# Optimization experiments

Hardware: AMD Instinct MI355X
Metric: run time of the kernel (lower is better)

Reference implementation:

```python
import jax, jax.numpy as jnp
import numpy as np
from functools import partial

T, B, I, H, L = 2048, 64, 256, 256, 3


def setup_inputs() -> dict:
    key = jax.random.key(0)
    ks = jax.random.split(key, 5)
    s = 1.0 / np.sqrt(H)  # PyTorch-style init scale
    x = jax.random.normal(ks[0], (T, B, I), dtype=jnp.float32)
    W_ih = jax.random.normal(ks[1], (L, 3 * H, I), dtype=jnp.float32) * s
    W_hh = jax.random.normal(ks[2], (L, 3 * H, H), dtype=jnp.float32) * s
    b_ih = jax.random.normal(ks[3], (L, 3 * H), dtype=jnp.float32) * s
    b_hh = jax.random.normal(ks[4], (L, 3 * H), dtype=jnp.float32) * s
    return {"x": x, "W_ih": W_ih, "W_hh": W_hh, "b_ih": b_ih, "b_hh": b_hh}


def _gru_layer(inp, Wi, Wh, bi, bh):
    # inp: [T, B, F]; Wi: [3H, F]; Wh: [3H, H]
    H_ = Wh.shape[1]
    # Precompute input-side gates for all timesteps (big GEMM outside scan).
    gi = jnp.einsum('tbf,gf->tbg', inp, Wi) + bi  # [T, B, 3H]

    def step(h, gi_t):
        gh = jnp.einsum('bh,gh->bg', h, Wh) + bh  # [B, 3H]
        i_r, i_z, i_n = jnp.split(gi_t, 3, axis=-1)
        h_r, h_z, h_n = jnp.split(gh, 3, axis=-1)
        r = jax.nn.sigmoid(i_r + h_r)
        z = jax.nn.sigmoid(i_z + h_z)
        n = jnp.tanh(i_n + r * h_n)
        h_new = (1.0 - z) * n + z * h
        return h_new, h_new

    h0 = jnp.zeros((inp.shape[1], H_), dtype=inp.dtype)
    _, out = jax.lax.scan(step, h0, gi)  # out: [T, B, H]
    return out


def reference(x, W_ih, W_hh, b_ih, b_hh):
    out = x
    for l in range(W_ih.shape[0]):  # fixed small layer count
        out = _gru_layer(out, W_ih[l], W_hh[l], b_ih[l], b_hh[l])
    return out[-1]  # [B, H] (last timestep of top layer)
```

## Files before the change

### kernel.cpp

```cpp
#include <hip/hip_runtime.h>
#include <cstdint>
#include <cstddef>

#define NT 2048
#define NB 64
#define NH 256
#define NG 768
#define NL 3
#define CHUNK 128
#define NCH (NT / CHUNK)

typedef _Float16 h2 __attribute__((ext_vector_type(2)));
union HU { unsigned int u; h2 h; };

__device__ __forceinline__ float sigf(float x) {
    return 1.0f / (1.0f + __expf(-x));
}
__device__ __forceinline__ float tanhfast(float x) {
    float e = __expf(2.0f * x);
    return 1.0f - 2.0f / (e + 1.0f);
}

__device__ __forceinline__ float dot8(uint4 wv, uint4 hv, float acc) {
#if __has_builtin(__builtin_amdgcn_fdot2)
    HU a, b;
    a.u = wv.x; b.u = hv.x; acc = __builtin_amdgcn_fdot2(a.h, b.h, acc, false);
    a.u = wv.y; b.u = hv.y; acc = __builtin_amdgcn_fdot2(a.h, b.h, acc, false);
    a.u = wv.z; b.u = hv.z; acc = __builtin_amdgcn_fdot2(a.h, b.h, acc, false);
    a.u = wv.w; b.u = hv.w; acc = __builtin_amdgcn_fdot2(a.h, b.h, acc, false);
#else
    HU a, b;
    const unsigned int wu[4] = {wv.x, wv.y, wv.z, wv.w};
    const unsigned int hu[4] = {hv.x, hv.y, hv.z, hv.w};
#pragma unroll
    for (int i = 0; i < 4; ++i) {
        a.u = wu[i]; b.u = hu[i];
        acc = fmaf((float)a.h[0], (float)b.h[0], acc);
        acc = fmaf((float)a.h[1], (float)b.h[1], acc);
    }
#endif
    return acc;
}

__global__ void repack_whh(const float* __restrict__ whh, uint4* __restrict__ wp) {
    int idx = blockIdx.x * 256 + threadIdx.x;
    if (idx >= NL * 48 * 512) return;
    int t  = idx & 511;
    int c  = (idx >> 9) % 48;
    int l  = idx / (48 * 512);
    int g  = c >> 4, cc = c & 15;
    int col = t >> 1, kh = t & 1;
    const float* row = whh + ((size_t)(l * NG + g * NH + col)) * NH + kh * 128 + cc * 8;
    HU u0, u1, u2, u3;
    u0.h = h2{(_Float16)row[0], (_Float16)row[1]};
    u1.h = h2{(_Float16)row[2], (_Float16)row[3]};
    u2.h = h2{(_Float16)row[4], (_Float16)row[5]};
    u3.h = h2{(_Float16)row[6], (_Float16)row[7]};
    wp[idx] = uint4{u0.u, u1.u, u2.u, u3.u};
}

__global__ __launch_bounds__(256) void gemm_gi(const float* __restrict__ A,
                                               const float* __restrict__ W,
                                               const float* __restrict__ bias,
                                               float* __restrict__ C) {
    __shared__ float As[32][68];
    __shared__ float Bs[32][68];
    const int tid = threadIdx.x;
    const int tx = tid & 15;
    const int ty = tid >> 4;
    const int m0 = blockIdx.y << 6;
    const int n0 = blockIdx.x << 6;
    const int lr = tid >> 2;
    const int lc = tid & 3;

    float acc[4][4] = {{0.0f}};

    for (int kt = 0; kt < 256; kt += 32) {
#pragma unroll
        for (int h = 0; h < 2; ++h) {
            const int c = lc + (h << 2);
            float4 av = *(const float4*)&A[(size_t)(m0 + lr) * 256 + kt + (c << 2)];
            float4 bv = *(const float4*)&W[(size_t)(n0 + lr) * 256 + kt + (c << 2)];
            As[(c << 2) + 0][lr] = av.x; As[(c << 2) + 1][lr] = av.y;
            As[(c << 2) + 2][lr] = av.z; As[(c << 2) + 3][lr] = av.w;
            Bs[(c << 2) + 0][lr] = bv.x; Bs[(c << 2) + 1][lr] = bv.y;
            Bs[(c << 2) + 2][lr] = bv.z; Bs[(c << 2) + 3][lr] = bv.w;
        }
        __syncthreads();
#pragma unroll
        for (int kk = 0; kk < 32; ++kk) {
            float4 a4 = *(const float4*)&As[kk][ty << 2];
            float4 b4 = *(const float4*)&Bs[kk][tx << 2];
            float a[4] = {a4.x, a4.y, a4.z, a4.w};
            float b[4] = {b4.x, b4.y, b4.z, b4.w};
#pragma unroll
            for (int i = 0; i < 4; ++i)
#pragma unroll
                for (int j = 0; j < 4; ++j)
                    acc[i][j] = fmaf(a[i], b[j], acc[i][j]);
        }
        __syncthreads();
    }

    const float4 bv = *(const float4*)&bias[n0 + (tx << 2)];
#pragma unroll
    for (int i = 0; i < 4; ++i) {
        float4 o;
        o.x = acc[i][0] + bv.x;
        o.y = acc[i][1] + bv.y;
        o.z = acc[i][2] + bv.z;
        o.w = acc[i][3] + bv.w;
        *(float4*)&C[(size_t)(m0 + (ty << 2) + i) * NG + n0 + (tx << 2)] = o;
    }
}

__global__ __launch_bounds__(512, 2) void gru_scan(const float* __restrict__ gi,
                                                   const uint4* __restrict__ wp,
                                                   const float* __restrict__ bh,
                                                   float* __restrict__ hst,
                                                   float* __restrict__ outf,
                                                   float* __restrict__ outl,
                                                   int steps) {
    const int b   = blockIdx.x;
    const int t   = threadIdx.x;
    const int col = t >> 1;
    const int kh  = t & 1;
    const bool own = (kh == 0);
    __shared__ __align__(16) _Float16 hsH[2][NH];

    uint4 w[48];
#pragma unroll
    for (int c = 0; c < 48; ++c) w[c] = wp[c * 512 + t];

    float h = hst[b * NH + col];
    const float bhr = bh[col];
    const float bhz = bh[NH + col];
    const float bhn = bh[2 * NH + col];

    if (own) hsH[0][col] = (_Float16)h;
    __syncthreads();

    const float* g0 = gi + (size_t)b * NG;
    float gr = g0[col], gz = g0[NH + col], gn = g0[2 * NH + col];

    int p = 0;
    for (int st = 0; st < steps; ++st) {
        const int stq = (st + 1 < steps) ? (st + 1) : st;
        const float* gq = gi + ((size_t)stq * NB + b) * NG;
        const float pr = gq[col], pz = gq[NH + col], pn = gq[2 * NH + col];

        const uint4* hv = (const uint4*)&hsH[p][kh << 7];
        float a0 = 0.0f, a1 = 0.0f, a2 = 0.0f;
#pragma unroll
        for (int cc = 0; cc < 16; ++cc) {
            const uint4 hh = hv[cc];
            a0 = dot8(w[cc],      hh, a0);
            a1 = dot8(w[16 + cc], hh, a1);
            a2 = dot8(w[32 + cc], hh, a2);
        }
        a0 += __shfl_xor(a0, 1);
        a1 += __shfl_xor(a1, 1);
        a2 += __shfl_xor(a2, 1);

        const float r = sigf(gr + a0 + bhr);
        const float z = sigf(gz + a1 + bhz);
        const float n = tanhfast(gn + r * (a2 + bhn));
        h = (1.0f - z) * n + z * h;

        if (own) {
            hsH[p ^ 1][col] = (_Float16)h;
            if (outf) outf[((size_t)st * NB + b) * NH + col] = h;
        }
        gr = pr; gz = pz; gn = pn;
        p ^= 1;
        __syncthreads();
    }

    if (own) {
        hst[b * NH + col] = h;
        if (outl) outl[b * NH + col] = h;
    }
}

extern "C" void kernel_launch(void* const* d_in, const int* in_sizes, int n_in,
                              void* d_out, int out_size, void* d_ws, size_t ws_size,
                              hipStream_t stream) {
    const float* x   = (const float*)d_in[0];
    const float* Wih = (const float*)d_in[1];
    const float* Whh = (const float*)d_in[2];
    const float* bih = (const float*)d_in[3];
    const float* bhh = (const float*)d_in[4];
    float* out = (float*)d_out;

    uint4* wpack = (uint4*)d_ws;
    float* hst = (float*)(wpack + NL * 48 * 512);
    float* gi  = hst + (size_t)NL * NB * NH;
    float* obA = gi + (size_t)CHUNK * NB * NG;
    float* obB = obA + (size_t)CHUNK * NB * NH;

    hipMemsetAsync(hst, 0, (size_t)NL * NB * NH * sizeof(float), stream);
    repack_whh<<<288, 256, 0, stream>>>(Whh, wpack);

    for (int c = 0; c < NCH; ++c) {
        for (int l = 0; l < NL; ++l) {
            const float* A = (l == 0) ? (x + (size_t)c * CHUNK * NB * NH)
                                      : ((l == 1) ? obA : obB);
            gemm_gi<<<dim3(12, CHUNK * NB / 64), 256, 0, stream>>>(
                A, Wih + (size_t)l * NG * NH, bih + (size_t)l * NG, gi);
            float* outf = (l == 0) ? obA : ((l == 1) ? obB : nullptr);
            float* outl = (l == 2 && c == NCH - 1) ? out : nullptr;
            gru_scan<<<NB, 512, 0, stream>>>(
                gi, wpack + (size_t)l * 48 * 512, bhh + (size_t)l * NG,
                hst + (size_t)l * NB * NH, outf, outl, CHUNK);
        }
    }
}
```

Baseline: 10.11 ms.

## Use fp16 MFMA for input GEMM and widen GRU scan to 1024 threads

Replaces the fp32 shared-memory SIMT GEMM for the input-side gates with an fp16 MFMA kernel that loads operands directly from global memory. Adds cast kernels that convert x and W_ih to fp16, and the scan now writes inter-layer activations in fp16. The recurrent scan splits each column's dot product across 4 threads instead of 2, giving 1024 threads per block and half as many weight registers per thread, with a padded shared-memory layout for h. The aim is to cut GEMM time and shorten the per-step serial latency, at the cost of extra fp16 rounding, an additional cross-lane reduction, and the cast kernel launches.

```diff
diff --git a/kernel.cpp b/kernel.cpp
--- a/kernel.cpp
+++ b/kernel.cpp
@@ -11,6 +11,8 @@
 #define NCH (NT / CHUNK)
 
 typedef _Float16 h2 __attribute__((ext_vector_type(2)));
+typedef _Float16 f16x8 __attribute__((ext_vector_type(8)));
+typedef float f32x4 __attribute__((ext_vector_type(4)));
 union HU { unsigned int u; h2 h; };
 
 __device__ __forceinline__ float sigf(float x) {
@@ -44,13 +46,13 @@
 
 __global__ void repack_whh(const float* __restrict__ whh, uint4* __restrict__ wp) {
     int idx = blockIdx.x * 256 + threadIdx.x;
-    if (idx >= NL * 48 * 512) return;
-    int t  = idx & 511;
-    int c  = (idx >> 9) % 48;
-    int l  = idx / (48 * 512);
-    int g  = c >> 4, cc = c & 15;
-    int col = t >> 1, kh = t & 1;
-    const float* row = whh + ((size_t)(l * NG + g * NH + col)) * NH + kh * 128 + cc * 8;
+    if (idx >= NL * 24 * 1024) return;
+    int t  = idx & 1023;
+    int c  = (idx >> 10) % 24;
+    int l  = idx / (24 * 1024);
+    int g  = c >> 3, cc = c & 7;
+    int col = t >> 2, kq = t & 3;
+    const float* row = whh + ((size_t)(l * NG + g * NH + col)) * NH + kq * 64 + cc * 8;
     HU u0, u1, u2, u3;
     u0.h = h2{(_Float16)row[0], (_Float16)row[1]};
     u1.h = h2{(_Float16)row[2], (_Float16)row[3]};
@@ -59,85 +61,81 @@
     wp[idx] = uint4{u0.u, u1.u, u2.u, u3.u};
 }
 
-__global__ __launch_bounds__(256) void gemm_gi(const float* __restrict__ A,
-                                               const float* __restrict__ W,
+__global__ void cast_f32_f16(const float* __restrict__ in, _Float16* __restrict__ outp,
+                             int n4) {
+    int i = blockIdx.x * 256 + threadIdx.x;
+    if (i >= n4) return;
+    float4 v = ((const float4*)in)[i];
+    h2 a = {(_Float16)v.x, (_Float16)v.y};
+    h2 b = {(_Float16)v.z, (_Float16)v.w};
+    HU ua, ub; ua.h = a; ub.h = b;
+    ((uint2*)outp)[i] = uint2{ua.u, ub.u};
+}
+
+__global__ __launch_bounds__(256) void gemm_gi(const _Float16* __restrict__ A,
+                                               const _Float16* __restrict__ W,
                                                const float* __restrict__ bias,
                                                float* __restrict__ C) {
-    __shared__ float As[32][68];
-    __shared__ float Bs[32][68];
-    const int tid = threadIdx.x;
-    const int tx = tid & 15;
-    const int ty = tid >> 4;
-    const int m0 = blockIdx.y << 6;
-    const int n0 = blockIdx.x << 6;
-    const int lr = tid >> 2;
-    const int lc = tid & 3;
-
-    float acc[4][4] = {{0.0f}};
-
-    for (int kt = 0; kt < 256; kt += 32) {
-#pragma unroll
-        for (int h = 0; h < 2; ++h) {
-            const int c = lc + (h << 2);
-            float4 av = *(const float4*)&A[(size_t)(m0 + lr) * 256 + kt + (c << 2)];
-            float4 bv = *(const float4*)&W[(size_t)(n0 + lr) * 256 + kt + (c << 2)];
-            As[(c << 2) + 0][lr] = av.x; As[(c << 2) + 1][lr] = av.y;
-            As[(c << 2) + 2][lr] = av.z; As[(c << 2) + 3][lr] = av.w;
-            Bs[(c << 2) + 0][lr] = bv.x; Bs[(c << 2) + 1][lr] = bv.y;
-            Bs[(c << 2) + 2][lr] = bv.z; Bs[(c << 2) + 3][lr] = bv.w;
-        }
-        __syncthreads();
-#pragma unroll
-        for (int kk = 0; kk < 32; ++kk) {
-            float4 a4 = *(const float4*)&As[kk][ty << 2];
-            float4 b4 = *(const float4*)&Bs[kk][tx << 2];
-            float a[4] = {a4.x, a4.y, a4.z, a4.w};
-            float b[4] = {b4.x, b4.y, b4.z, b4.w};
-#pragma unroll
-            for (int i = 0; i < 4; ++i)
-#pragma unroll
-                for (int j = 0; j < 4; ++j)
-                    acc[i][j] = fmaf(a[i], b[j], acc[i][j]);
-        }
-        __syncthreads();
-    }
-
-    const float4 bv = *(const float4*)&bias[n0 + (tx << 2)];
-#pragma unroll
-    for (int i = 0; i < 4; ++i) {
-        float4 o;
-        o.x = acc[i][0] + bv.x;
-        o.y = acc[i][1] + bv.y;
-        o.z = acc[i][2] + bv.z;
-        o.w = acc[i][3] + bv.w;
-        *(float4*)&C[(size_t)(m0 + (ty << 2) + i) * NG + n0 + (tx << 2)] = o;
-    }
-}
-
-__global__ __launch_bounds__(512, 2) void gru_scan(const float* __restrict__ gi,
-                                                   const uint4* __restrict__ wp,
-                                                   const float* __restrict__ bh,
-                                                   float* __restrict__ hst,
-                                                   float* __restrict__ outf,
-                                                   float* __restrict__ outl,
-                                                   int steps) {
+    const int lane = threadIdx.x & 63;
+    const int wv   = threadIdx.x >> 6;
+    const int m0   = (blockIdx.y << 6) + (wv << 4);
+    const int n0   = blockIdx.x << 6;
+    const int r    = lane & 15;
+    const int ko   = (lane >> 4) << 3;
+
+    const _Float16* arow = A + (size_t)(m0 + r) * NH + ko;
+    const _Float16* wrow = W + (size_t)(n0 + r) * NH + ko;
+
+    f32x4 acc0 = {0,0,0,0}, acc1 = {0,0,0,0}, acc2 = {0,0,0,0}, acc3 = {0,0,0,0};
+#pragma unroll
+    for (int k0 = 0; k0 < 8; ++k0) {
+        const f16x8 af = *(const f16x8*)(arow + k0 * 32);
+        const f16x8 b0 = *(const f16x8*)(wrow + k0 * 32);
+        const f16x8 b1 = *(const f16x8*)(wrow + 16 * NH + k0 * 32);
+        const f16x8 b2 = *(const f16x8*)(wrow + 32 * NH + k0 * 32);
+        const f16x8 b3 = *(const f16x8*)(wrow + 48 * NH + k0 * 32);
+        acc0 = __builtin_amdgcn_mfma_f32_16x16x32_f16(af, b0, acc0, 0, 0, 0);
+        acc1 = __builtin_amdgcn_mfma_f32_16x16x32_f16(af, b1, acc1, 0, 0, 0);
+        acc2 = __builtin_amdgcn_mfma_f32_16x16x32_f16(af, b2, acc2, 0, 0, 0);
+        acc3 = __builtin_amdgcn_mfma_f32_16x16x32_f16(af, b3, acc3, 0, 0, 0);
+    }
+
+    const int rowb = m0 + ((lane >> 4) << 2);
+    const f32x4 av[4] = {acc0, acc1, acc2, acc3};
+#pragma unroll
+    for (int j = 0; j < 4; ++j) {
+        const int col = n0 + (j << 4) + r;
+        const float bb = bias[col];
+#pragma unroll
+        for (int q = 0; q < 4; ++q)
+            C[(size_t)(rowb + q) * NG + col] = av[j][q] + bb;
+    }
+}
+
+__global__ __launch_bounds__(1024, 4) void gru_scan(const float* __restrict__ gi,
+                                                    const uint4* __restrict__ wp,
+                                                    const float* __restrict__ bh,
+                                                    float* __restrict__ hst,
+                                                    _Float16* __restrict__ outf,
+                                                    float* __restrict__ outl,
+                                                    int steps) {
     const int b   = blockIdx.x;
     const int t   = threadIdx.x;
-    const int col = t >> 1;
-    const int kh  = t & 1;
-    const bool own = (kh == 0);
-    __shared__ __align__(16) _Float16 hsH[2][NH];
-
-    uint4 w[48];
-#pragma unroll
-    for (int c = 0; c < 48; ++c) w[c] = wp[c * 512 + t];
+    const int col = t >> 2;
+    const int kq  = t & 3;
+    const bool own = (kq == 0);
+    __shared__ __align__(16) unsigned char hraw[2][576];
+
+    uint4 w[24];
+#pragma unroll
+    for (int c = 0; c < 24; ++c) w[c] = wp[c * 1024 + t];
 
     float h = hst[b * NH + col];
     const float bhr = bh[col];
     const float bhz = bh[NH + col];
     const float bhn = bh[2 * NH + col];
 
-    if (own) hsH[0][col] = (_Float16)h;
+    if (own) *(_Float16*)&hraw[0][(col >> 6) * 144 + (col & 63) * 2] = (_Float16)h;
     __syncthreads();
 
     const float* g0 = gi + (size_t)b * NG;
@@ -149,18 +147,18 @@
         const float* gq = gi + ((size_t)stq * NB + b) * NG;
         const float pr = gq[col], pz = gq[NH + col], pn = gq[2 * NH + col];
 
-        const uint4* hv = (const uint4*)&hsH[p][kh << 7];
+        const uint4* hv = (const uint4*)&hraw[p][kq * 144];
         float a0 = 0.0f, a1 = 0.0f, a2 = 0.0f;
 #pragma unroll
-        for (int cc = 0; cc < 16; ++cc) {
+        for (int cc = 0; cc < 8; ++cc) {
             const uint4 hh = hv[cc];
             a0 = dot8(w[cc],      hh, a0);
-            a1 = dot8(w[16 + cc], hh, a1);
-            a2 = dot8(w[32 + cc], hh, a2);
+            a1 = dot8(w[8 + cc],  hh, a1);
+            a2 = dot8(w[16 + cc], hh, a2);
         }
-        a0 += __shfl_xor(a0, 1);
-        a1 += __shfl_xor(a1, 1);
-        a2 += __shfl_xor(a2, 1);
+        a0 += __shfl_xor(a0, 1); a0 += __shfl_xor(a0, 2);
+        a1 += __shfl_xor(a1, 1); a1 += __shfl_xor(a1, 2);
+        a2 += __shfl_xor(a2, 1); a2 += __shfl_xor(a2, 2);
 
         const float r = sigf(gr + a0 + bhr);
         const float z = sigf(gz + a1 + bhz);
@@ -168,8 +166,8 @@
         h = (1.0f - z) * n + z * h;
 
         if (own) {
-            hsH[p ^ 1][col] = (_Float16)h;
-            if (outf) outf[((size_t)st * NB + b) * NH + col] = h;
+            *(_Float16*)&hraw[p ^ 1][(col >> 6) * 144 + (col & 63) * 2] = (_Float16)h;
+            if (outf) outf[((size_t)st * NB + b) * NH + col] = (_Float16)h;
         }
         gr = pr; gz = pz; gn = pn;
         p ^= 1;
@@ -192,25 +190,29 @@
     const float* bhh = (const float*)d_in[4];
     float* out = (float*)d_out;
 
-    uint4* wpack = (uint4*)d_ws;
-    float* hst = (float*)(wpack + NL * 48 * 512);
-    float* gi  = hst + (size_t)NL * NB * NH;
-    float* obA = gi + (size_t)CHUNK * NB * NG;
-    float* obB = obA + (size_t)CHUNK * NB * NH;
+    uint4*     wpack = (uint4*)d_ws;
+    float*     gi    = (float*)(wpack + NL * 24 * 1024);
+    float*     hst   = gi + (size_t)CHUNK * NB * NG;
+    _Float16*  xh    = (_Float16*)(hst + (size_t)NL * NB * NH);
+    _Float16*  obA   = xh + (size_t)CHUNK * NB * NH;
+    _Float16*  obB   = obA + (size_t)CHUNK * NB * NH;
+    _Float16*  wihh  = obB + (size_t)CHUNK * NB * NH;
 
     hipMemsetAsync(hst, 0, (size_t)NL * NB * NH * sizeof(float), stream);
     repack_whh<<<288, 256, 0, stream>>>(Whh, wpack);
+    cast_f32_f16<<<576, 256, 0, stream>>>(Wih, wihh, NL * NG * NH / 4);
 
     for (int c = 0; c < NCH; ++c) {
+        cast_f32_f16<<<2048, 256, 0, stream>>>(
+            x + (size_t)c * CHUNK * NB * NH, xh, CHUNK * NB * NH / 4);
         for (int l = 0; l < NL; ++l) {
-            const float* A = (l == 0) ? (x + (size_t)c * CHUNK * NB * NH)
-                                      : ((l == 1) ? obA : obB);
+            const _Float16* A = (l == 0) ? xh : ((l == 1) ? obA : obB);
             gemm_gi<<<dim3(12, CHUNK * NB / 64), 256, 0, stream>>>(
-                A, Wih + (size_t)l * NG * NH, bih + (size_t)l * NG, gi);
-            float* outf = (l == 0) ? obA : ((l == 1) ? obB : nullptr);
+                A, wihh + (size_t)l * NG * NH, bih + (size_t)l * NG, gi);
+            _Float16* outf = (l == 0) ? obA : ((l == 1) ? obB : nullptr);
             float* outl = (l == 2 && c == NCH - 1) ? out : nullptr;
-            gru_scan<<<NB, 512, 0, stream>>>(
-                gi, wpack + (size_t)l * 48 * 512, bhh + (size_t)l * NG,
+            gru_scan<<<NB, 1024, 0, stream>>>(
+                gi, wpack + (size_t)l * 24 * 1024, bhh + (size_t)l * NG,
                 hst + (size_t)l * NB * NH, outf, outl, CHUNK);
         }
     }
```

Result: slower. 11.80 ms (+16.7%).
